# Optimization experiments

Hardware: AMD Instinct MI355X
Metric: run time of the kernel (lower is better)

Reference implementation:

```python
import jax, jax.numpy as jnp
import numpy as np

H = 20  # hidden size (hardcoded in the torch module)

def setup_inputs() -> dict:
    key = jax.random.key(0)
    ks = jax.random.split(key, 7)
    s = 0.1  # keep activations in a sane range for tanh/sigmoid
    return {
        "x":     jax.random.normal(ks[0], (8192, 512, 12), dtype=jnp.float32),
        "w_ih":  jax.random.normal(ks[1], (4 * H, 12), dtype=jnp.float32) * s,
        "w_hh":  jax.random.normal(ks[2], (4 * H, H), dtype=jnp.float32) * s,
        "b_ih":  jax.random.normal(ks[3], (4 * H,), dtype=jnp.float32) * s,
        "b_hh":  jax.random.normal(ks[4], (4 * H,), dtype=jnp.float32) * s,
        "w_out": jax.random.normal(ks[5], (10, H), dtype=jnp.float32) * s,
        "b_out": jax.random.normal(ks[6], (10,), dtype=jnp.float32) * s,
    }

def reference(x, w_ih, w_hh, b_ih, b_hh, w_out, b_out):
    # x: [B, T, I]. Single-layer LSTM (PyTorch gate order i,f,g,o), zero init state,
    # then Linear on the last hidden state.
    B, T, _ = x.shape
    # Precompute input projections for all timesteps: [T, B, 4H]
    x_proj = jnp.einsum('bti,gi->tbg', x, w_ih) + (b_ih + b_hh)

    def step(carry, xt):
        h, c = carry                      # each [B, H]
        gates = xt + h @ w_hh.T           # [B, 4H]
        i, f, g, o = jnp.split(gates, 4, axis=-1)
        i = jax.nn.sigmoid(i)
        f = jax.nn.sigmoid(f)
        g = jnp.tanh(g)
        o = jax.nn.sigmoid(o)
        c = f * c + i * g
        h = o * jnp.tanh(c)
        return (h, c), None

    h0 = jnp.zeros((B, H), dtype=x.dtype)
    c0 = jnp.zeros((B, H), dtype=x.dtype)
    (h_last, _), _ = jax.lax.scan(step, (h0, c0), x_proj)
    # out = Linear(h_T): r_out[:, -1, :] == h_n for a single-layer LSTM
    return h_last @ w_out.T + b_out
```

## Files before the change

kernel.cpp:

```cpp
#include <hip/hip_runtime.h>

typedef _Float16 f16;
typedef f16 f16x8 __attribute__((ext_vector_type(8)));
typedef float f32x4 __attribute__((ext_vector_type(4)));

#define T_STEPS 512
#define INPUT   12
#define HID     20
#define KDIM    32
#define BSTRIDE 40
#define BATCH   16
#define WPB     5
#define BLOCK   (WPB * 64)

static __device__ __forceinline__ void block_barrier() {
    asm volatile("s_waitcnt lgkmcnt(0)\n\ts_barrier" ::: "memory");
}

static __device__ __forceinline__ float fast_sigmoid(float x) {
    float e = __builtin_amdgcn_exp2f(-1.4426950408889634f * x);
    return __builtin_amdgcn_rcpf(1.0f + e);
}
static __device__ __forceinline__ float fast_tanh(float x) {
    float e = __builtin_amdgcn_exp2f(2.8853900817779268f * x);
    return 1.0f - 2.0f * __builtin_amdgcn_rcpf(1.0f + e);
}

__global__ __launch_bounds__(BLOCK) void lstm_kernel(
    const float* __restrict__ x,
    const float* __restrict__ w_ih,
    const float* __restrict__ w_hh,
    const float* __restrict__ b_ih,
    const float* __restrict__ b_hh,
    const float* __restrict__ w_out,
    const float* __restrict__ b_out,
    float* __restrict__ out)
{
    __shared__ __align__(16) f16 Wc[80][KDIM];
    __shared__ __align__(16) f16 Bbuf[2][BATCH][BSTRIDE];

    const int tid  = threadIdx.x;
    const int wid  = tid >> 6;
    const int lane = tid & 63;
    const int col  = lane & 15;
    const int quad = lane >> 4;

    for (int i = tid; i < 80 * KDIM; i += BLOCK) {
        int n = i >> 5, k = i & 31;
        int g = n & 3;
        int u = 4 * (n >> 4) + ((n >> 2) & 3);
        int row = g * HID + u;
        float v = (k < INPUT) ? w_ih[row * INPUT + k] : w_hh[row * HID + (k - INPUT)];
        Wc[n][k] = (f16)v;
    }

    const int b = col;
    const int u = 4 * wid + quad;

    f32x4 cbias;
#pragma unroll
    for (int g = 0; g < 4; ++g)
        cbias[g] = b_ih[g * HID + u] + b_hh[g * HID + u];

    Bbuf[0][b][INPUT + u] = (f16)0.f;

    const bool xload = tid < BATCH * INPUT;
    const int  xb    = tid / INPUT;
    const int  xi    = tid % INPUT;
    const float* xptr = x + (size_t)(blockIdx.x * BATCH + xb) * (T_STEPS * INPUT) + xi;

    float xv = 0.f;
    if (xload) {
        Bbuf[0][xb][xi] = (f16)xptr[0];
        xv = xptr[INPUT];
    }
    __syncthreads();

    const f16x8 afragW = *(const f16x8*)&Wc[16 * wid + col][quad * 8];

    float cc = 0.f;
    int p = 0;

#pragma unroll 1
    for (int t = 0; t < T_STEPS; ++t) {
        f16x8 bfrag = *(const f16x8*)&Bbuf[p][col][quad * 8];

        if (xload) Bbuf[p ^ 1][xb][xi] = (f16)xv;
        int tn = t + 2; if (tn > T_STEPS - 1) tn = T_STEPS - 1;
        if (xload) xv = xptr[(size_t)tn * INPUT];

        f32x4 acc = __builtin_amdgcn_mfma_f32_16x16x32_f16(afragW, bfrag, cbias, 0, 0, 0);

        float ig = fast_sigmoid(acc[0]);
        float fg = fast_sigmoid(acc[1]);
        float gt = fast_tanh(acc[2]);
        float og = fast_sigmoid(acc[3]);
        cc = fg * cc + ig * gt;
        float h = og * fast_tanh(cc);

        Bbuf[p ^ 1][b][INPUT + u] = (f16)h;
        block_barrier();
        p ^= 1;
    }

    if (tid < BATCH * 10) {
        int ob = tid / 10, oo = tid % 10;
        float s = b_out[oo];
#pragma unroll
        for (int u2 = 0; u2 < HID; ++u2)
            s += w_out[oo * HID + u2] * (float)Bbuf[0][ob][INPUT + u2];
        out[(size_t)(blockIdx.x * BATCH + ob) * 10 + oo] = s;
    }
}

extern "C" void kernel_launch(void* const* d_in, const int* in_sizes, int n_in,
                              void* d_out, int out_size, void* d_ws, size_t ws_size,
                              hipStream_t stream) {
    const float* x     = (const float*)d_in[0];
    const float* w_ih  = (const float*)d_in[1];
    const float* w_hh  = (const float*)d_in[2];
    const float* b_ih  = (const float*)d_in[3];
    const float* b_hh  = (const float*)d_in[4];
    const float* w_out = (const float*)d_in[5];
    const float* b_out = (const float*)d_in[6];
    float* out = (float*)d_out;

    const int blocks = 8192 / BATCH;
    hipLaunchKernelGGL(lstm_kernel, dim3(blocks), dim3(BLOCK), 0, stream,
                       x, w_ih, w_hh, b_ih, b_hh, w_out, b_out, out);
}
```

Measured before the change: 428.2 us.

## Run each batch tile's LSTM recurrence in a single wave with register-resident state

The recurrence moves from five waves sharing hidden state through LDS with a block barrier every step to one wave per 16-sequence block. That wave issues five MFMAs per step and rebuilds its B fragment in registers, exploiting that the MFMA output layout matches the next step's K-slot assignment. The activation scale factors (log2e) are folded into the weights and biases, and x is loaded as unaligned float4 with double-buffered prefetch. The aim is to remove the per-step LDS round trip and barrier. The cost is that each wave now does five times the MFMA and transcendental work serially, and 512 single-wave blocks may leave much of the GPU idle.

Measured after the change: 444.3 us. 1.04x slower.

```diff
diff --git a/kernel.cpp b/kernel.cpp
--- a/kernel.cpp
+++ b/kernel.cpp
@@ -1,32 +1,31 @@
 #include <hip/hip_runtime.h>
 
 typedef _Float16 f16;
-typedef f16 f16x8 __attribute__((ext_vector_type(8)));
-typedef float f32x4 __attribute__((ext_vector_type(4)));
+typedef f16   f16x2  __attribute__((ext_vector_type(2)));
+typedef f16   f16x8  __attribute__((ext_vector_type(8)));
+typedef float f32x4  __attribute__((ext_vector_type(4)));
+typedef float f32x4u __attribute__((ext_vector_type(4), aligned(4)));
+typedef __fp16 h16x2 __attribute__((ext_vector_type(2)));
 
 #define T_STEPS 512
 #define INPUT   12
 #define HID     20
-#define KDIM    32
-#define BSTRIDE 40
 #define BATCH   16
-#define WPB     5
-#define BLOCK   (WPB * 64)
+#define LOG2E      1.4426950408889634f
+#define TWO_LOG2E  2.8853900817779268f
 
-static __device__ __forceinline__ void block_barrier() {
-    asm volatile("s_waitcnt lgkmcnt(0)\n\ts_barrier" ::: "memory");
+static __device__ __forceinline__ f16x2 pk(float a, float b) {
+    h16x2 r = __builtin_amdgcn_cvt_pkrtz(a, b);
+    return __builtin_bit_cast(f16x2, r);
+}
+static __device__ __forceinline__ float sig_pre(float a) {
+    return __builtin_amdgcn_rcpf(1.0f + __builtin_amdgcn_exp2f(a));
+}
+static __device__ __forceinline__ float tanh_pre(float a) {
+    return 1.0f - 2.0f * __builtin_amdgcn_rcpf(1.0f + __builtin_amdgcn_exp2f(a));
 }
 
-static __device__ __forceinline__ float fast_sigmoid(float x) {
-    float e = __builtin_amdgcn_exp2f(-1.4426950408889634f * x);
-    return __builtin_amdgcn_rcpf(1.0f + e);
-}
-static __device__ __forceinline__ float fast_tanh(float x) {
-    float e = __builtin_amdgcn_exp2f(2.8853900817779268f * x);
-    return 1.0f - 2.0f * __builtin_amdgcn_rcpf(1.0f + e);
-}
-
-__global__ __launch_bounds__(BLOCK) void lstm_kernel(
+__global__ __launch_bounds__(64) void lstm_kernel(
     const float* __restrict__ x,
     const float* __restrict__ w_ih,
     const float* __restrict__ w_hh,
@@ -36,80 +35,120 @@
     const float* __restrict__ b_out,
     float* __restrict__ out)
 {
-    __shared__ __align__(16) f16 Wc[80][KDIM];
-    __shared__ __align__(16) f16 Bbuf[2][BATCH][BSTRIDE];
-
-    const int tid  = threadIdx.x;
-    const int wid  = tid >> 6;
-    const int lane = tid & 63;
+    const int lane = threadIdx.x & 63;
     const int col  = lane & 15;
     const int quad = lane >> 4;
 
-    for (int i = tid; i < 80 * KDIM; i += BLOCK) {
-        int n = i >> 5, k = i & 31;
-        int g = n & 3;
-        int u = 4 * (n >> 4) + ((n >> 2) & 3);
-        int row = g * HID + u;
-        float v = (k < INPUT) ? w_ih[row * INPUT + k] : w_hh[row * HID + (k - INPUT)];
-        Wc[n][k] = (f16)v;
+    const int   g_row = col & 3;
+    const float sA    = (g_row == 2) ? TWO_LOG2E : -LOG2E;
+
+    f16x8 afragW[5];
+#pragma unroll
+    for (int t = 0; t < 5; ++t) {
+        int u_r = 5 * (col >> 2) + t;
+        int row = g_row * HID + u_r;
+        f16x8 w;
+#pragma unroll
+        for (int j = 0; j < 8; ++j) {
+            float v = (j < 3) ? w_ih[row * INPUT + 3 * quad + j]
+                              : w_hh[row * HID + 5 * quad + (j - 3)];
+            w[j] = (f16)(v * sA);
+        }
+        afragW[t] = w;
     }
 
-    const int b = col;
-    const int u = 4 * wid + quad;
+    f32x4 cbias[5];
+#pragma unroll
+    for (int t = 0; t < 5; ++t) {
+        int u_b = 5 * quad + t;
+#pragma unroll
+        for (int r = 0; r < 4; ++r) {
+            float s = (r == 2) ? TWO_LOG2E : -LOG2E;
+            cbias[t][r] = (b_ih[r * HID + u_b] + b_hh[r * HID + u_b]) * s;
+        }
+    }
 
-    f32x4 cbias;
+    const int al_words = (quad == 0) ? 0 : (quad == 1) ? 2 : (quad == 2) ? 6 : 8;
+    const int sel      = quad & 1;
+    const float* xp = x + (size_t)(blockIdx.x * BATCH + col) * (T_STEPS * INPUT) + al_words;
+
+    auto loadx = [&](int t) -> f32x4 {
+        return *(const f32x4u*)(xp + (size_t)t * INPUT);
+    };
+
+    union BF { f16x8 v; f16x2 h2[4]; } bf;
+    {
+        f32x4 xv = loadx(0);
+        float x0 = sel ? xv[1] : xv[0];
+        float x1 = sel ? xv[2] : xv[1];
+        float x2 = sel ? xv[3] : xv[2];
+        bf.h2[0] = pk(x0, x1);
+        bf.h2[1] = pk(x2, 0.f);
+        bf.h2[2] = pk(0.f, 0.f);
+        bf.h2[3] = pk(0.f, 0.f);
+    }
+
+    float cst[5] = {0.f, 0.f, 0.f, 0.f, 0.f};
+
+    f32x4 qA = loadx(1);
+    f32x4 qB = loadx(2);
+
+    auto step = [&](f32x4& q, int tl) {
+        f32x4 acc[5];
 #pragma unroll
-    for (int g = 0; g < 4; ++g)
-        cbias[g] = b_ih[g * HID + u] + b_hh[g * HID + u];
+        for (int t = 0; t < 5; ++t)
+            acc[t] = __builtin_amdgcn_mfma_f32_16x16x32_f16(afragW[t], bf.v, cbias[t], 0, 0, 0);
 
-    Bbuf[0][b][INPUT + u] = (f16)0.f;
+        float h[5];
+#pragma unroll
+        for (int t = 0; t < 5; ++t) {
+            float ig = sig_pre(acc[t][0]);
+            float fg = sig_pre(acc[t][1]);
+            float gg = tanh_pre(acc[t][2]);
+            float og = sig_pre(acc[t][3]);
+            float c2 = fg * cst[t] + ig * gg;
+            cst[t] = c2;
+            h[t] = og * tanh_pre(TWO_LOG2E * c2);
+        }
 
-    const bool xload = tid < BATCH * INPUT;
-    const int  xb    = tid / INPUT;
-    const int  xi    = tid % INPUT;
-    const float* xptr = x + (size_t)(blockIdx.x * BATCH + xb) * (T_STEPS * INPUT) + xi;
+        float x0 = sel ? q[1] : q[0];
+        float x1 = sel ? q[2] : q[1];
+        float x2 = sel ? q[3] : q[2];
+        q = loadx(tl);
 
-    float xv = 0.f;
-    if (xload) {
-        Bbuf[0][xb][xi] = (f16)xptr[0];
-        xv = xptr[INPUT];
+        bf.h2[0] = pk(x0, x1);
+        bf.h2[1] = pk(x2, h[0]);
+        bf.h2[2] = pk(h[1], h[2]);
+        bf.h2[3] = pk(h[3], h[4]);
+    };
+
+#pragma unroll 1
+    for (int t = 0; t < T_STEPS; t += 2) {
+        int l1 = t + 3; if (l1 > T_STEPS - 1) l1 = T_STEPS - 1;
+        int l2 = t + 4; if (l2 > T_STEPS - 1) l2 = T_STEPS - 1;
+        step(qA, l1);
+        step(qB, l2);
     }
+
+    __shared__ f16 htmp[BATCH][HID];
+    htmp[col][5 * quad + 0] = bf.h2[1][1];
+    htmp[col][5 * quad + 1] = bf.h2[2][0];
+    htmp[col][5 * quad + 2] = bf.h2[2][1];
+    htmp[col][5 * quad + 3] = bf.h2[3][0];
+    htmp[col][5 * quad + 4] = bf.h2[3][1];
     __syncthreads();
 
-    const f16x8 afragW = *(const f16x8*)&Wc[16 * wid + col][quad * 8];
-
-    float cc = 0.f;
-    int p = 0;
-
-#pragma unroll 1
-    for (int t = 0; t < T_STEPS; ++t) {
-        f16x8 bfrag = *(const f16x8*)&Bbuf[p][col][quad * 8];
-
-        if (xload) Bbuf[p ^ 1][xb][xi] = (f16)xv;
-        int tn = t + 2; if (tn > T_STEPS - 1) tn = T_STEPS - 1;
-        if (xload) xv = xptr[(size_t)tn * INPUT];
-
-        f32x4 acc = __builtin_amdgcn_mfma_f32_16x16x32_f16(afragW, bfrag, cbias, 0, 0, 0);
-
-        float ig = fast_sigmoid(acc[0]);
-        float fg = fast_sigmoid(acc[1]);
-        float gt = fast_tanh(acc[2]);
-        float og = fast_sigmoid(acc[3]);
-        cc = fg * cc + ig * gt;
-        float h = og * fast_tanh(cc);
-
-        Bbuf[p ^ 1][b][INPUT + u] = (f16)h;
-        block_barrier();
-        p ^= 1;
-    }
-
-    if (tid < BATCH * 10) {
-        int ob = tid / 10, oo = tid % 10;
-        float s = b_out[oo];
 #pragma unroll
-        for (int u2 = 0; u2 < HID; ++u2)
-            s += w_out[oo * HID + u2] * (float)Bbuf[0][ob][INPUT + u2];
-        out[(size_t)(blockIdx.x * BATCH + ob) * 10 + oo] = s;
+    for (int base = 0; base < BATCH * 10; base += 64) {
+        int idx = base + lane;
+        if (idx < BATCH * 10) {
+            int b = idx / 10, o = idx % 10;
+            float s = b_out[o];
+#pragma unroll
+            for (int u = 0; u < HID; ++u)
+                s += (float)htmp[b][u] * w_out[o * HID + u];
+            out[(size_t)(blockIdx.x * BATCH + b) * 10 + o] = s;
+        }
     }
 }
 
@@ -126,6 +165,6 @@
     float* out = (float*)d_out;
 
     const int blocks = 8192 / BATCH;
-    hipLaunchKernelGGL(lstm_kernel, dim3(blocks), dim3(BLOCK), 0, stream,
+    hipLaunchKernelGGL(lstm_kernel, dim3(blocks), dim3(64), 0, stream,
                        x, w_ih, w_hh, b_ih, b_hh, w_out, b_out, out);
 }
```
